# Kernel optimization log

Hardware: AMD Instinct MI355X
Metric: run time of the kernel (lower is better)

Reference implementation:

```python
import jax, jax.numpy as jnp
import numpy as np

N, K, F = 50000, 16, 128
ALPHA = 0.2
NEG_INF = -9e15


def setup_inputs() -> dict:
    key = jax.random.key(0)
    k1, k2, k3, k4, k5 = jax.random.split(key, 5)
    orignal_x = jax.random.normal(k1, (N, F), dtype=jnp.float32)
    x = jax.random.normal(k2, (N, K, F), dtype=jnp.float32)
    adj = jax.random.randint(k3, (N, K), 0, 2, dtype=jnp.int32)
    # xavier-uniform-ish params
    limW = np.sqrt(6.0 / (F + F)) * 1.414
    W = jax.random.uniform(k4, (F, F), dtype=jnp.float32, minval=-limW, maxval=limW)
    lima = np.sqrt(6.0 / (2 * F + 1)) * 1.414
    a = jax.random.uniform(k5, (2 * F, 1), dtype=jnp.float32, minval=-lima, maxval=lima)
    return {"orignal_x": orignal_x, "x": x, "adj": adj, "W": W, "a": a}


def reference(orignal_x, x, adj, W, a):
    # h: [N, F] projected self features
    h = orignal_x @ W
    # h_j: [N, K, F] projected neighbor (anchor) features
    h_j = jnp.einsum('nkf,fo->nko', x, W)
    # split attention vector instead of materializing concat([h_i, h_j])
    a1 = a[:F, 0]   # [F]
    a2 = a[F:, 0]   # [F]
    scores = h @ a1                      # [N]
    scores = scores[:, None] + h_j @ a2  # [N, K]
    e = jax.nn.leaky_relu(scores, negative_slope=ALPHA)
    e = jnp.where(adj > 0, e, NEG_INF)
    attention = jax.nn.softmax(e, axis=1)           # [N, K]
    # dropout is identity in eval mode
    h_prime = jnp.einsum('nk,nkf->nf', attention, h_j)
    h_prime = h_prime + h  # args.attentionAddSelf assumed True
    return jax.nn.elu(h_prime)  # concat=True -> elu; nheads=1 -> [N, F]
```

## Files before the change

kernel.cpp:

```cpp
#include <hip/hip_runtime.h>

#define NN 50000
#define KK 16
#define FF 128
#define NB 32
#define NW 8
#define NEGI -9.0e15f

typedef float fx4 __attribute__((ext_vector_type(4)));
typedef float fx2 __attribute__((ext_vector_type(2)));

template <int CTRL>
__device__ __forceinline__ float dpp_add(float v) {
  int s = __builtin_amdgcn_mov_dpp(__float_as_int(v), CTRL, 0xF, 0xF, true);
  return v + __int_as_float(s);
}
template <int PAT>
__device__ __forceinline__ float swz_add(float v) {
  int s = __builtin_amdgcn_ds_swizzle(__float_as_int(v), PAT);
  return v + __int_as_float(s);
}
__device__ __forceinline__ float red32(float v) {
  v = dpp_add<0xB1>(v);
  v = dpp_add<0x4E>(v);
  v = dpp_add<0x141>(v);
  v = dpp_add<0x140>(v);
  v = swz_add<0x401F>(v);
  return v;
}
__device__ __forceinline__ float dot4(float4 a, float4 b) {
  return fmaf(a.x, b.x, fmaf(a.y, b.y, fmaf(a.z, b.z, a.w * b.w)));
}
__device__ __forceinline__ float4 ntload4(const float* p) {
  fx4 v = __builtin_nontemporal_load((const fx4*)p);
  return make_float4(v.x, v.y, v.z, v.w);
}

__global__ void gat_pre(const float* __restrict__ Wm, const float* __restrict__ Av,
                        const int* __restrict__ ADJ, float* __restrict__ wa_out,
                        unsigned* __restrict__ msk_out) {
  const int tid = threadIdx.x;
  const int gi = blockIdx.x * 256 + tid;
  if (gi < NN * 4) {
    const int4 a = ((const int4*)ADJ)[gi];
    unsigned nib = (unsigned)(a.x > 0) | ((unsigned)(a.y > 0) << 1) |
                   ((unsigned)(a.z > 0) << 2) | ((unsigned)(a.w > 0) << 3);
    unsigned v = nib << (4 * (gi & 3));
    v |= (unsigned)__shfl_xor((int)v, 1);
    v |= (unsigned)__shfl_xor((int)v, 2);
    if ((gi & 3) == 0) msk_out[gi >> 2] = v;
  }
  if (blockIdx.x == 0) {
    const int f = tid & 127, sel = tid >> 7;
    const float4* W4 = (const float4*)(Wm + f * FF);
    const float4* A4 = (const float4*)(Av + sel * FF);
    float s = 0.f;
#pragma unroll
    for (int u = 0; u < 32; ++u) {
      float4 wv = W4[u], av = A4[u];
      s += wv.x * av.x + wv.y * av.y + wv.z * av.z + wv.w * av.w;
    }
    wa_out[tid] = s;
  }
}

__global__ __launch_bounds__(256, 2)
void gat_fused(const float* __restrict__ OX, const float* __restrict__ X,
               const unsigned* __restrict__ MSK, const float* __restrict__ WA,
               const float* __restrict__ Wm, float* __restrict__ out) {
  __shared__ float xs[4 * 8 * 132];

  const int tid  = threadIdx.x;
  const int l    = tid & 63;
  const int j    = l & 31;
  const int half = l >> 5;
  const int wu   = __builtin_amdgcn_readfirstlane(tid >> 6);
  const int nbase = blockIdx.x * NB + wu * NW;
  float* xsw = xs + wu * (8 * 132);

  const float4 w1 = ((const float4*)WA)[j];
  const float4 w2 = ((const float4*)WA)[32 + j];

  const int limit = (NN - nbase < NW) ? (NN - nbase) : NW;

  unsigned mks[NW];
#pragma unroll
  for (int i = 0; i < NW; ++i) mks[i] = (i < limit) ? MSK[nbase + i] : 0u;

  auto PRELOAD = [&](int i, float4* xv, float4& ox) {
    const int n = nbase + i;
    const unsigned ml = mks[i] ? mks[i] : 0xFFFFu;
    const float* xp = X + (size_t)n * (KK * FF);
#pragma unroll
    for (int t = 0; t < 8; ++t) {
      xv[t] = make_float4(0.f, 0.f, 0.f, 0.f);
      if ((ml >> (2 * t + half)) & 1u)
        xv[t] = ntload4(xp + (t * 64 + l) * 4);
    }
    ox = ntload4(OX + (size_t)n * FF + j * 4);
  };

  auto PROCA = [&](int i, const float4* xv, float4 ox) {
    const unsigned mk = mks[i];
    const float s0 = red32(dot4(ox, w1));
    float e[8];
#pragma unroll
    for (int t = 0; t < 8; ++t) e[t] = red32(dot4(xv[t], w2)) + s0;

    float m = -3.0e38f;
#pragma unroll
    for (int t = 0; t < 8; ++t) {
      float v = e[t];
      v = fmaxf(v, 0.2f * v);
      e[t] = ((mk >> (2 * t + half)) & 1u) ? v : NEGI;
      m = fmaxf(m, e[t]);
    }
    m = fmaxf(m, __shfl_xor(m, 32));

    float ss = 0.f;
    float4 pacc = {0.f, 0.f, 0.f, 0.f};
#pragma unroll
    for (int t = 0; t < 8; ++t) {
      const float w = __expf(e[t] - m);
      ss += w;
      pacc.x = fmaf(w, xv[t].x, pacc.x);
      pacc.y = fmaf(w, xv[t].y, pacc.y);
      pacc.z = fmaf(w, xv[t].z, pacc.z);
      pacc.w = fmaf(w, xv[t].w, pacc.w);
    }
    ss += __shfl_xor(ss, 32);
    pacc.x += __shfl_xor(pacc.x, 32);
    pacc.y += __shfl_xor(pacc.y, 32);
    pacc.z += __shfl_xor(pacc.z, 32);
    pacc.w += __shfl_xor(pacc.w, 32);
    const float inv = 1.0f / ss;

    float4 xa;
    xa.x = fmaf(inv, pacc.x, ox.x);
    xa.y = fmaf(inv, pacc.y, ox.y);
    xa.z = fmaf(inv, pacc.z, ox.z);
    xa.w = fmaf(inv, pacc.w, ox.w);

    if (half == 0)
      *(float4*)&xsw[i * 132 + j * 4] = xa;
  };

  {
    float4 xva[8], xvb[8], xvc[8], xvd[8];
    float4 oxa, oxb, oxc, oxd;
    if (0 < limit) PRELOAD(0, xva, oxa);
    if (1 < limit) PRELOAD(1, xvb, oxb);
    if (2 < limit) PRELOAD(2, xvc, oxc);
    if (3 < limit) PRELOAD(3, xvd, oxd);

    if (0 < limit) PROCA(0, xva, oxa);
    if (4 < limit) PRELOAD(4, xva, oxa);
    if (1 < limit) PROCA(1, xvb, oxb);
    if (5 < limit) PRELOAD(5, xvb, oxb);
    if (2 < limit) PROCA(2, xvc, oxc);
    if (6 < limit) PRELOAD(6, xvc, oxc);
    if (3 < limit) PROCA(3, xvd, oxd);
    if (7 < limit) PRELOAD(7, xvd, oxd);

    if (4 < limit) PROCA(4, xva, oxa);
    if (5 < limit) PROCA(5, xvb, oxb);
    if (6 < limit) PROCA(6, xvc, oxc);
    if (7 < limit) PROCA(7, xvd, oxd);
  }

  float2 acc[NW];
#pragma unroll
  for (int i = 0; i < NW; ++i) { acc[i].x = 0.f; acc[i].y = 0.f; }

#pragma unroll 4
  for (int q = 0; q < 32; ++q) {
    const float* wr = Wm + (size_t)(4 * q) * FF;
    const float2 wv0 = ((const float2*)(wr))[l];
    const float2 wv1 = ((const float2*)(wr + FF))[l];
    const float2 wv2 = ((const float2*)(wr + 2 * FF))[l];
    const float2 wv3 = ((const float2*)(wr + 3 * FF))[l];
#pragma unroll
    for (int i = 0; i < NW; ++i) {
      const float4 xa4 = *(const float4*)&xsw[i * 132 + q * 4];
      acc[i].x = fmaf(xa4.x, wv0.x, fmaf(xa4.y, wv1.x, fmaf(xa4.z, wv2.x, fmaf(xa4.w, wv3.x, acc[i].x))));
      acc[i].y = fmaf(xa4.x, wv0.y, fmaf(xa4.y, wv1.y, fmaf(xa4.z, wv2.y, fmaf(xa4.w, wv3.y, acc[i].y))));
    }
  }

#pragma unroll
  for (int i = 0; i < NW; ++i) {
    const int n2 = nbase + i;
    if (i < limit) {
      fx2 st;
      st.x = acc[i].x > 0.f ? acc[i].x : (__expf(acc[i].x) - 1.0f);
      st.y = acc[i].y > 0.f ? acc[i].y : (__expf(acc[i].y) - 1.0f);
      __builtin_nontemporal_store(st, (fx2*)(out + (size_t)n2 * FF) + l);
    }
  }
}

extern "C" void kernel_launch(void* const* d_in, const int* in_sizes, int n_in,
                              void* d_out, int out_size, void* d_ws, size_t ws_size,
                              hipStream_t stream) {
  const float* OX  = (const float*)d_in[0];
  const float* X   = (const float*)d_in[1];
  const int*   ADJ = (const int*)d_in[2];
  const float* Wm  = (const float*)d_in[3];
  const float* Av  = (const float*)d_in[4];
  float* out = (float*)d_out;
  float* wa  = (float*)d_ws;
  unsigned* msk = (unsigned*)d_ws + 256;

  const int preblocks = (NN * 4 + 255) / 256;
  gat_pre<<<preblocks, 256, 0, stream>>>(Wm, Av, ADJ, wa, msk);
  const int blocks = (NN + NB - 1) / NB;
  gat_fused<<<blocks, 256, 0, stream>>>(OX, X, msk, wa, Wm, out);
}
```

Measured before the change: 89.70 us.

## Split fused GAT kernel into attention and output projection kernels

Splits the single fused kernel in two. The first computes the attention-weighted aggregate plus the self term and writes it to a workspace buffer in global memory. The second reads that buffer back into shared memory, applies the W projection and ELU, and declares higher occupancy in its launch bounds. The aim is to decouple the memory-bound attention phase from the compute-bound matmul phase, so each can run at better occupancy and overlap better. The cost is an extra round trip through global memory for an N×F intermediate (about 25.6 MB written and read) and one more kernel launch.

```diff
diff --git a/kernel.cpp b/kernel.cpp
--- a/kernel.cpp
+++ b/kernel.cpp
@@ -65,18 +65,15 @@
 }
 
 __global__ __launch_bounds__(256, 2)
-void gat_fused(const float* __restrict__ OX, const float* __restrict__ X,
-               const unsigned* __restrict__ MSK, const float* __restrict__ WA,
-               const float* __restrict__ Wm, float* __restrict__ out) {
-  __shared__ float xs[4 * 8 * 132];
-
+void gat_attn(const float* __restrict__ OX, const float* __restrict__ X,
+              const unsigned* __restrict__ MSK, const float* __restrict__ WA,
+              float* __restrict__ XA) {
   const int tid  = threadIdx.x;
   const int l    = tid & 63;
   const int j    = l & 31;
   const int half = l >> 5;
   const int wu   = __builtin_amdgcn_readfirstlane(tid >> 6);
   const int nbase = blockIdx.x * NB + wu * NW;
-  float* xsw = xs + wu * (8 * 132);
 
   const float4 w1 = ((const float4*)WA)[j];
   const float4 w2 = ((const float4*)WA)[32 + j];
@@ -101,6 +98,7 @@
   };
 
   auto PROCA = [&](int i, const float4* xv, float4 ox) {
+    const int n = nbase + i;
     const unsigned mk = mks[i];
     const float s0 = red32(dot4(ox, w1));
     float e[8];
@@ -142,30 +140,51 @@
     xa.w = fmaf(inv, pacc.w, ox.w);
 
     if (half == 0)
-      *(float4*)&xsw[i * 132 + j * 4] = xa;
+      *(float4*)(XA + (size_t)n * FF + 4 * j) = xa;
   };
 
-  {
-    float4 xva[8], xvb[8], xvc[8], xvd[8];
-    float4 oxa, oxb, oxc, oxd;
-    if (0 < limit) PRELOAD(0, xva, oxa);
-    if (1 < limit) PRELOAD(1, xvb, oxb);
-    if (2 < limit) PRELOAD(2, xvc, oxc);
-    if (3 < limit) PRELOAD(3, xvd, oxd);
-
-    if (0 < limit) PROCA(0, xva, oxa);
-    if (4 < limit) PRELOAD(4, xva, oxa);
-    if (1 < limit) PROCA(1, xvb, oxb);
-    if (5 < limit) PRELOAD(5, xvb, oxb);
-    if (2 < limit) PROCA(2, xvc, oxc);
-    if (6 < limit) PRELOAD(6, xvc, oxc);
-    if (3 < limit) PROCA(3, xvd, oxd);
-    if (7 < limit) PRELOAD(7, xvd, oxd);
-
-    if (4 < limit) PROCA(4, xva, oxa);
-    if (5 < limit) PROCA(5, xvb, oxb);
-    if (6 < limit) PROCA(6, xvc, oxc);
-    if (7 < limit) PROCA(7, xvd, oxd);
+  float4 xva[8], xvb[8], xvc[8], xvd[8];
+  float4 oxa, oxb, oxc, oxd;
+  if (0 < limit) PRELOAD(0, xva, oxa);
+  if (1 < limit) PRELOAD(1, xvb, oxb);
+  if (2 < limit) PRELOAD(2, xvc, oxc);
+  if (3 < limit) PRELOAD(3, xvd, oxd);
+
+  if (0 < limit) PROCA(0, xva, oxa);
+  if (4 < limit) PRELOAD(4, xva, oxa);
+  if (1 < limit) PROCA(1, xvb, oxb);
+  if (5 < limit) PRELOAD(5, xvb, oxb);
+  if (2 < limit) PROCA(2, xvc, oxc);
+  if (6 < limit) PRELOAD(6, xvc, oxc);
+  if (3 < limit) PROCA(3, xvd, oxd);
+  if (7 < limit) PRELOAD(7, xvd, oxd);
+
+  if (4 < limit) PROCA(4, xva, oxa);
+  if (5 < limit) PROCA(5, xvb, oxb);
+  if (6 < limit) PROCA(6, xvc, oxc);
+  if (7 < limit) PROCA(7, xvd, oxd);
+}
+
+__global__ __launch_bounds__(256, 4)
+void gat_out(const float* __restrict__ XA, const float* __restrict__ Wm,
+             float* __restrict__ out) {
+  __shared__ float xs[4][1024];
+
+  const int tid = threadIdx.x;
+  const int l   = tid & 63;
+  const int wu  = __builtin_amdgcn_readfirstlane(tid >> 6);
+  const int nbase = blockIdx.x * NB + wu * NW;
+  float* xsw = xs[wu];
+
+  const int limit = (NN - nbase < NW) ? (NN - nbase) : NW;
+  if (limit <= 0) return;
+
+  const float4* src = (const float4*)(XA + (size_t)nbase * FF);
+  const int nq = limit * 32;
+#pragma unroll
+  for (int c = 0; c < 4; ++c) {
+    const int idx = c * 64 + l;
+    if (idx < nq) ((float4*)xsw)[idx] = src[idx];
   }
 
   float2 acc[NW];
@@ -181,7 +200,7 @@
     const float2 wv3 = ((const float2*)(wr + 3 * FF))[l];
 #pragma unroll
     for (int i = 0; i < NW; ++i) {
-      const float4 xa4 = *(const float4*)&xsw[i * 132 + q * 4];
+      const float4 xa4 = ((const float4*)xsw)[i * 32 + q];
       acc[i].x = fmaf(xa4.x, wv0.x, fmaf(xa4.y, wv1.x, fmaf(xa4.z, wv2.x, fmaf(xa4.w, wv3.x, acc[i].x))));
       acc[i].y = fmaf(xa4.x, wv0.y, fmaf(xa4.y, wv1.y, fmaf(xa4.z, wv2.y, fmaf(xa4.w, wv3.y, acc[i].y))));
     }
@@ -189,12 +208,11 @@
 
 #pragma unroll
   for (int i = 0; i < NW; ++i) {
-    const int n2 = nbase + i;
     if (i < limit) {
       fx2 st;
       st.x = acc[i].x > 0.f ? acc[i].x : (__expf(acc[i].x) - 1.0f);
       st.y = acc[i].y > 0.f ? acc[i].y : (__expf(acc[i].y) - 1.0f);
-      __builtin_nontemporal_store(st, (fx2*)(out + (size_t)n2 * FF) + l);
+      __builtin_nontemporal_store(st, (fx2*)(out + (size_t)(nbase + i) * FF) + l);
     }
   }
 }
@@ -210,9 +228,11 @@
   float* out = (float*)d_out;
   float* wa  = (float*)d_ws;
   unsigned* msk = (unsigned*)d_ws + 256;
+  float* XA = (float*)d_ws + 65536;
 
   const int preblocks = (NN * 4 + 255) / 256;
   gat_pre<<<preblocks, 256, 0, stream>>>(Wm, Av, ADJ, wa, msk);
   const int blocks = (NN + NB - 1) / NB;
-  gat_fused<<<blocks, 256, 0, stream>>>(OX, X, msk, wa, Wm, out);
-}
+  gat_attn<<<blocks, 256, 0, stream>>>(OX, X, msk, wa, XA);
+  gat_out<<<blocks, 256, 0, stream>>>(XA, Wm, out);
+}
```

New measurement: 105.4 us. +17.5%, slower.

## Fold adjacency mask building into fused kernel and halve nodes per wave

Applied to the files above, without the earlier changes.

Mask packing moves out of the pre-kernel and into the fused kernel: each wave loads its 4 nodes' adjacency rows and builds per-node bitmasks with cross-lane shuffles. This removes the separate mask pass and its global round trip, so the pre-kernel shrinks to a single block computing W·a. Nodes per wave drop from 8 to 4 with a single preload/process stage, which gives more blocks but less in-wave overlap of loads with compute. Bounds checks are removed because 50000 divides evenly by 16.

```diff
diff --git a/kernel.cpp b/kernel.cpp
--- a/kernel.cpp
+++ b/kernel.cpp
@@ -3,8 +3,8 @@
 #define NN 50000
 #define KK 16
 #define FF 128
-#define NB 32
-#define NW 8
+#define NB 16
+#define NW 4
 #define NEGI -9.0e15f
 
 typedef float fx4 __attribute__((ext_vector_type(4)));
@@ -36,39 +36,26 @@
   return make_float4(v.x, v.y, v.z, v.w);
 }
 
-__global__ void gat_pre(const float* __restrict__ Wm, const float* __restrict__ Av,
-                        const int* __restrict__ ADJ, float* __restrict__ wa_out,
-                        unsigned* __restrict__ msk_out) {
+__global__ void gat_wa(const float* __restrict__ Wm, const float* __restrict__ Av,
+                       float* __restrict__ wa_out) {
   const int tid = threadIdx.x;
-  const int gi = blockIdx.x * 256 + tid;
-  if (gi < NN * 4) {
-    const int4 a = ((const int4*)ADJ)[gi];
-    unsigned nib = (unsigned)(a.x > 0) | ((unsigned)(a.y > 0) << 1) |
-                   ((unsigned)(a.z > 0) << 2) | ((unsigned)(a.w > 0) << 3);
-    unsigned v = nib << (4 * (gi & 3));
-    v |= (unsigned)__shfl_xor((int)v, 1);
-    v |= (unsigned)__shfl_xor((int)v, 2);
-    if ((gi & 3) == 0) msk_out[gi >> 2] = v;
+  const int f = tid & 127, sel = tid >> 7;
+  const float4* W4 = (const float4*)(Wm + f * FF);
+  const float4* A4 = (const float4*)(Av + sel * FF);
+  float s = 0.f;
+#pragma unroll
+  for (int u = 0; u < 32; ++u) {
+    float4 wv = W4[u], av = A4[u];
+    s += wv.x * av.x + wv.y * av.y + wv.z * av.z + wv.w * av.w;
   }
-  if (blockIdx.x == 0) {
-    const int f = tid & 127, sel = tid >> 7;
-    const float4* W4 = (const float4*)(Wm + f * FF);
-    const float4* A4 = (const float4*)(Av + sel * FF);
-    float s = 0.f;
-#pragma unroll
-    for (int u = 0; u < 32; ++u) {
-      float4 wv = W4[u], av = A4[u];
-      s += wv.x * av.x + wv.y * av.y + wv.z * av.z + wv.w * av.w;
-    }
-    wa_out[tid] = s;
-  }
+  wa_out[tid] = s;
 }
 
 __global__ __launch_bounds__(256, 2)
 void gat_fused(const float* __restrict__ OX, const float* __restrict__ X,
-               const unsigned* __restrict__ MSK, const float* __restrict__ WA,
+               const int* __restrict__ ADJ, const float* __restrict__ WA,
                const float* __restrict__ Wm, float* __restrict__ out) {
-  __shared__ float xs[4 * 8 * 132];
+  __shared__ float xs[4 * 4 * 132];
 
   const int tid  = threadIdx.x;
   const int l    = tid & 63;
@@ -76,18 +63,29 @@
   const int half = l >> 5;
   const int wu   = __builtin_amdgcn_readfirstlane(tid >> 6);
   const int nbase = blockIdx.x * NB + wu * NW;
-  float* xsw = xs + wu * (8 * 132);
+  float* xsw = xs + wu * (NW * 132);
+
+  const int adjv = ADJ[nbase * KK + l];
+  float4 ox0 = ntload4(OX + (size_t)(nbase + 0) * FF + 4 * j);
+  float4 ox1 = ntload4(OX + (size_t)(nbase + 1) * FF + 4 * j);
+  float4 ox2 = ntload4(OX + (size_t)(nbase + 2) * FF + 4 * j);
+  float4 ox3 = ntload4(OX + (size_t)(nbase + 3) * FF + 4 * j);
 
   const float4 w1 = ((const float4*)WA)[j];
   const float4 w2 = ((const float4*)WA)[32 + j];
 
-  const int limit = (NN - nbase < NW) ? (NN - nbase) : NW;
+  unsigned b = (adjv > 0) ? (1u << (l & 15)) : 0u;
+  b |= (unsigned)__shfl_xor((int)b, 1);
+  b |= (unsigned)__shfl_xor((int)b, 2);
+  b |= (unsigned)__shfl_xor((int)b, 4);
+  b |= (unsigned)__shfl_xor((int)b, 8);
+  unsigned mks[NW];
+  mks[0] = (unsigned)__shfl((int)b, 0);
+  mks[1] = (unsigned)__shfl((int)b, 16);
+  mks[2] = (unsigned)__shfl((int)b, 32);
+  mks[3] = (unsigned)__shfl((int)b, 48);
 
-  unsigned mks[NW];
-#pragma unroll
-  for (int i = 0; i < NW; ++i) mks[i] = (i < limit) ? MSK[nbase + i] : 0u;
-
-  auto PRELOAD = [&](int i, float4* xv, float4& ox) {
+  auto PRELOAD = [&](int i, float4* xv) {
     const int n = nbase + i;
     const unsigned ml = mks[i] ? mks[i] : 0xFFFFu;
     const float* xp = X + (size_t)n * (KK * FF);
@@ -97,7 +95,6 @@
       if ((ml >> (2 * t + half)) & 1u)
         xv[t] = ntload4(xp + (t * 64 + l) * 4);
     }
-    ox = ntload4(OX + (size_t)n * FF + j * 4);
   };
 
   auto PROCA = [&](int i, const float4* xv, float4 ox) {
@@ -147,25 +144,14 @@
 
   {
     float4 xva[8], xvb[8], xvc[8], xvd[8];
-    float4 oxa, oxb, oxc, oxd;
-    if (0 < limit) PRELOAD(0, xva, oxa);
-    if (1 < limit) PRELOAD(1, xvb, oxb);
-    if (2 < limit) PRELOAD(2, xvc, oxc);
-    if (3 < limit) PRELOAD(3, xvd, oxd);
-
-    if (0 < limit) PROCA(0, xva, oxa);
-    if (4 < limit) PRELOAD(4, xva, oxa);
-    if (1 < limit) PROCA(1, xvb, oxb);
-    if (5 < limit) PRELOAD(5, xvb, oxb);
-    if (2 < limit) PROCA(2, xvc, oxc);
-    if (6 < limit) PRELOAD(6, xvc, oxc);
-    if (3 < limit) PROCA(3, xvd, oxd);
-    if (7 < limit) PRELOAD(7, xvd, oxd);
-
-    if (4 < limit) PROCA(4, xva, oxa);
-    if (5 < limit) PROCA(5, xvb, oxb);
-    if (6 < limit) PROCA(6, xvc, oxc);
-    if (7 < limit) PROCA(7, xvd, oxd);
+    PRELOAD(0, xva);
+    PRELOAD(1, xvb);
+    PRELOAD(2, xvc);
+    PRELOAD(3, xvd);
+    PROCA(0, xva, ox0);
+    PROCA(1, xvb, ox1);
+    PROCA(2, xvc, ox2);
+    PROCA(3, xvd, ox3);
   }
 
   float2 acc[NW];
@@ -189,13 +175,10 @@
 
 #pragma unroll
   for (int i = 0; i < NW; ++i) {
-    const int n2 = nbase + i;
-    if (i < limit) {
-      fx2 st;
-      st.x = acc[i].x > 0.f ? acc[i].x : (__expf(acc[i].x) - 1.0f);
-      st.y = acc[i].y > 0.f ? acc[i].y : (__expf(acc[i].y) - 1.0f);
-      __builtin_nontemporal_store(st, (fx2*)(out + (size_t)n2 * FF) + l);
-    }
+    fx2 st;
+    st.x = acc[i].x > 0.f ? acc[i].x : (__expf(acc[i].x) - 1.0f);
+    st.y = acc[i].y > 0.f ? acc[i].y : (__expf(acc[i].y) - 1.0f);
+    __builtin_nontemporal_store(st, (fx2*)(out + (size_t)(nbase + i) * FF) + l);
   }
 }
 
@@ -209,10 +192,7 @@
   const float* Av  = (const float*)d_in[4];
   float* out = (float*)d_out;
   float* wa  = (float*)d_ws;
-  unsigned* msk = (unsigned*)d_ws + 256;
 
-  const int preblocks = (NN * 4 + 255) / 256;
-  gat_pre<<<preblocks, 256, 0, stream>>>(Wm, Av, ADJ, wa, msk);
-  const int blocks = (NN + NB - 1) / NB;
-  gat_fused<<<blocks, 256, 0, stream>>>(OX, X, msk, wa, Wm, out);
+  gat_wa<<<1, 256, 0, stream>>>(Wm, Av, wa);
+  gat_fused<<<NN / NB, 256, 0, stream>>>(OX, X, ADJ, wa, Wm, out);
 }
```

After: 97.18 us. 8.3% more time.
